# Kernel optimization log

Measured on AMD Instinct MI355X. Metric: run time of the kernel, lower is better.

Reference implementation:

```python
import jax, jax.numpy as jnp
import numpy as np

B, C_IN, C_OUT, N, MODES = 16, 128, 128, 16384, 128

def setup_inputs() -> dict:
    key = jax.random.key(0)
    k1, k2, k3, k4 = jax.random.split(key, 4)
    scale = 1.0 / (C_IN * C_OUT)
    x = jax.random.normal(k1, (B, C_IN, N), dtype=jnp.float32)
    wbases = jax.random.normal(k2, (N, MODES), dtype=jnp.float32)
    bases = jax.random.normal(k3, (N, MODES), dtype=jnp.float32)
    W = scale * jax.random.uniform(k4, (C_IN, C_OUT, MODES), dtype=jnp.float32)
    return {"x": x, "wbases": wbases, "bases": bases, "W": W}

def reference(x, wbases, bases, W):
    # project onto weighted bases: [B, C_in, N] x [N, K] -> [B, C_in, K]
    x_co = jnp.einsum('bcx,xk->bck', x, wbases)
    # per-mode channel mixing: [B, C_in, K] x [C_in, C_out, K] -> [B, C_out, K]
    x_hat = jnp.einsum('bik,iok->bok', x_co, W)
    # reconstruct: [B, C_out, K] x [N, K] -> [B, C_out, N]
    return jnp.einsum('bok,xk->box', x_hat, bases)
```

## Files before the change

### kernel.cpp

```cpp
#include <hip/hip_runtime.h>
#include <hip/hip_bf16.h>
#include <stdint.h>

#define NB 16
#define NC 128
#define NK 128
#define NSP 16384
#define SPLIT 32
#define CHUNK 512
#define BK 64

typedef float f32x4 __attribute__((ext_vector_type(4)));
typedef __bf16 bf16x8 __attribute__((ext_vector_type(8)));

__device__ __forceinline__ unsigned short f32_to_bf16(float a) {
  unsigned int u = __float_as_uint(a);
  return (unsigned short)((u + 0x7fffu + ((u >> 16) & 1u)) >> 16);
}

__device__ __forceinline__ unsigned int pack_bf16(float a, float b) {
  unsigned int ua = __float_as_uint(a);
  unsigned int ub = __float_as_uint(b);
  ua = (ua + 0x7fffu + ((ua >> 16) & 1u)) >> 16;
  ub = (ub + 0x7fffu + ((ub >> 16) & 1u)) & 0xffff0000u;
  return ua | ub;
}

__device__ __forceinline__ bf16x8 pack8(float4 a0, float4 a1) {
  uint4 u;
  u.x = pack_bf16(a0.x, a0.y);
  u.y = pack_bf16(a0.z, a0.w);
  u.z = pack_bf16(a1.x, a1.y);
  u.w = pack_bf16(a1.z, a1.w);
  return __builtin_bit_cast(bf16x8, u);
}

__global__ void k0_prep(const float* __restrict__ wb, unsigned short* __restrict__ wbT,
                        const float* __restrict__ bases, unsigned short* __restrict__ bb) {
  __shared__ float tile[32][33];
  if (blockIdx.x < 2048) {
    int bid = blockIdx.x;
    int kt = (bid & 3) * 32;
    int nt = (bid >> 2) * 32;
    int tx = threadIdx.x & 31;
    int ty = threadIdx.x >> 5;
#pragma unroll
    for (int i = 0; i < 32; i += 8)
      tile[ty + i][tx] = wb[(size_t)(nt + ty + i) * NK + kt + tx];
    __syncthreads();
#pragma unroll
    for (int i = 0; i < 32; i += 8)
      wbT[(size_t)(kt + ty + i) * NSP + nt + tx] = f32_to_bf16(tile[tx][ty + i]);
  } else {
    int i = (blockIdx.x - 2048) * 256 + threadIdx.x;
    float4 v = ((const float4*)bases)[i];
    uint2 o;
    o.x = pack_bf16(v.x, v.y);
    o.y = pack_bf16(v.z, v.w);
    ((uint2*)bb)[i] = o;
  }
}

__global__ __launch_bounds__(256, 4)
void k1_proj(const float* __restrict__ x, const unsigned short* __restrict__ wbT,
             float* __restrict__ part) {
  int blk = blockIdx.x;
  int khalf = blk >> 9;
  int b = (blk >> 5) & 15;
  int chunk = blk & 31;
  int n0 = chunk * CHUNK;
  int tid = threadIdx.x;
  int lane = tid & 63;
  int wave = tid >> 6;
  int cb = (wave & 1) * 64;
  int kb = khalf * 64 + (wave >> 1) * 32;
  int r = lane & 15;
  int q = lane >> 4;

  f32x4 acc[4][2];
#pragma unroll
  for (int t = 0; t < 4; ++t)
#pragma unroll
    for (int u = 0; u < 2; ++u) acc[t][u] = (f32x4){0.f, 0.f, 0.f, 0.f};

  const float* xrow = x + (size_t)(b * NC + cb + r) * NSP + n0;
  const unsigned short* wrow = wbT + (size_t)(kb + r) * NSP + n0;

#pragma unroll 2
  for (int it = 0; it < CHUNK / BK; ++it) {
#pragma unroll
    for (int s = 0; s < 2; ++s) {
      int c2 = it * BK + s * 32 + q * 8;
      bf16x8 af[4], bf[2];
#pragma unroll
      for (int t = 0; t < 4; ++t) {
        const float4* p = (const float4*)(xrow + (size_t)t * 16 * NSP + c2);
        af[t] = pack8(p[0], p[1]);
      }
#pragma unroll
      for (int u = 0; u < 2; ++u)
        bf[u] = *(const bf16x8*)(wrow + (size_t)u * 16 * NSP + c2);
#pragma unroll
      for (int t = 0; t < 4; ++t)
#pragma unroll
        for (int u = 0; u < 2; ++u)
          acc[t][u] = __builtin_amdgcn_mfma_f32_16x16x32_bf16(af[t], bf[u],
                                                              acc[t][u], 0, 0, 0);
    }
  }

  float* pp = part + (size_t)(b * SPLIT + chunk) * (NC * NK);
  int rq = q * 4;
#pragma unroll
  for (int t = 0; t < 4; ++t)
#pragma unroll
    for (int u = 0; u < 2; ++u)
#pragma unroll
      for (int v = 0; v < 4; ++v)
        pp[(cb + 16 * t + rq + v) * NK + kb + 16 * u + r] = acc[t][u][v];
}

__global__ __launch_bounds__(256)
void k1b_reduce(const float* __restrict__ part, float* __restrict__ x_co) {
  int idx = blockIdx.x * 256 + threadIdx.x;
  int b = idx >> 13;
  int r2 = idx & 8191;
  const float2* p = (const float2*)(part + (size_t)b * SPLIT * (NC * NK)) + r2;
  float2 s = {0.f, 0.f};
#pragma unroll
  for (int c = 0; c < SPLIT; ++c) {
    float2 v = p[(size_t)c * (NC * NK / 2)];
    s.x += v.x;
    s.y += v.y;
  }
  ((float2*)x_co)[idx] = s;
}

__global__ __launch_bounds__(128)
void k2_mix(const float* __restrict__ x_co, const float* __restrict__ W,
            unsigned short* __restrict__ xhat_bf) {
  int b = blockIdx.x >> 6;
  int o0 = (blockIdx.x & 63) * 2;
  int k = threadIdx.x;
  const float* xc = x_co + (size_t)b * NC * NK + k;
  const float* w0 = W + (size_t)o0 * NK + k;
  float a0 = 0.f, a1 = 0.f;
#pragma unroll 4
  for (int i = 0; i < NC; ++i) {
    float v = xc[(size_t)i * NK];
    a0 += v * w0[(size_t)i * (NC * NK)];
    a1 += v * w0[(size_t)i * (NC * NK) + NK];
  }
  size_t base = ((size_t)b * NC + o0) * NK + k;
  xhat_bf[base] = f32_to_bf16(a0);
  xhat_bf[base + NK] = f32_to_bf16(a1);
}

__global__ __launch_bounds__(256, 4)
void k3_recon(const unsigned short* __restrict__ xhat_bf,
              const unsigned short* __restrict__ bases_bf,
              float* __restrict__ out) {
  int blk = blockIdx.x;
  int mo0 = (blk & 15) * 128;
  int n0 = (blk >> 4) * 256;
  int tid = threadIdx.x;
  int lane = tid & 63;
  int wave = tid >> 6;
  int mb = (wave & 1) * 64;
  int nb = (wave >> 1) * 64;
  int r = lane & 15;
  int q = lane >> 4;
  int rq = q * 4;

  const unsigned short* arow = xhat_bf + (size_t)(mo0 + mb + r) * NK + q * 8;

#pragma unroll
  for (int sub = 0; sub < 2; ++sub) {
    const unsigned short* brow =
        bases_bf + (size_t)(n0 + sub * 128 + nb + r) * NK + q * 8;
    f32x4 acc[4][4];
#pragma unroll
    for (int t = 0; t < 4; ++t)
#pragma unroll
      for (int u = 0; u < 4; ++u) acc[t][u] = (f32x4){0.f, 0.f, 0.f, 0.f};
#pragma unroll
    for (int s = 0; s < 4; ++s) {
      bf16x8 af[4], bf[4];
#pragma unroll
      for (int t = 0; t < 4; ++t)
        af[t] = *(const bf16x8*)(arow + (size_t)t * 16 * NK + s * 32);
#pragma unroll
      for (int u = 0; u < 4; ++u)
        bf[u] = *(const bf16x8*)(brow + (size_t)u * 16 * NK + s * 32);
#pragma unroll
      for (int t = 0; t < 4; ++t)
#pragma unroll
        for (int u = 0; u < 4; ++u)
          acc[t][u] = __builtin_amdgcn_mfma_f32_16x16x32_bf16(af[t], bf[u],
                                                              acc[t][u], 0, 0, 0);
    }
    float* obase = out + (size_t)(mo0 + mb + rq) * NSP + n0 + sub * 128 + nb + r;
#pragma unroll
    for (int t = 0; t < 4; ++t)
#pragma unroll
      for (int u = 0; u < 4; ++u)
#pragma unroll
        for (int v = 0; v < 4; ++v)
          obase[(size_t)(16 * t + v) * NSP + 16 * u] = acc[t][u][v];
  }
}

extern "C" void kernel_launch(void* const* d_in, const int* in_sizes, int n_in,
                              void* d_out, int out_size, void* d_ws, size_t ws_size,
                              hipStream_t stream) {
  const float* x = (const float*)d_in[0];
  const float* wbases = (const float*)d_in[1];
  const float* bases = (const float*)d_in[2];
  const float* W = (const float*)d_in[3];
  float* out = (float*)d_out;

  char* ws = (char*)d_ws;
  if (ws_size < ((size_t)42 << 20)) return;
  unsigned short* wbT = (unsigned short*)(ws);
  unsigned short* bases_bf = (unsigned short*)(ws + ((size_t)4 << 20));
  float* part = (float*)(ws + ((size_t)8 << 20));
  float* x_co = (float*)(ws + ((size_t)40 << 20));
  unsigned short* xhat_bf = (unsigned short*)(ws + ((size_t)41 << 20));

  k0_prep<<<4096, 256, 0, stream>>>(wbases, wbT, bases, bases_bf);
  k1_proj<<<1024, 256, 0, stream>>>(x, wbT, part);
  k1b_reduce<<<512, 256, 0, stream>>>(part, x_co);
  k2_mix<<<NB * NC / 2, 128, 0, stream>>>(x_co, W, xhat_bf);
  k3_recon<<<1024, 256, 0, stream>>>(xhat_bf, bases_bf, out);
}
```

Measured before the change: 360.7 us.

## Stage k1 projection tiles through double-buffered LDS via direct global-to-LDS loads

Reworks the projection kernel so each block covers half the input channels and all 128 modes, so the x data is read once instead of twice across mode halves. Tiles of x (fp32, XOR-swizzled) and bf16 wbases are copied into a double-buffered LDS area with global_load_lds, and the next tile is prefetched while MFMAs run on the current one. The change adds a block barrier every 32-element step and converts fp32 to bf16 when reading from LDS. It also uses 32KB of LDS per block, which may reduce occupancy.

```diff
diff --git a/kernel.cpp b/kernel.cpp
--- a/kernel.cpp
+++ b/kernel.cpp
@@ -8,7 +8,6 @@
 #define NSP 16384
 #define SPLIT 32
 #define CHUNK 512
-#define BK 64
 
 typedef float f32x4 __attribute__((ext_vector_type(4)));
 typedef __bf16 bf16x8 __attribute__((ext_vector_type(8)));
@@ -33,6 +32,12 @@
   u.z = pack_bf16(a1.x, a1.y);
   u.w = pack_bf16(a1.z, a1.w);
   return __builtin_bit_cast(bf16x8, u);
+}
+
+__device__ __forceinline__ void gl_lds16(const void* g, void* l) {
+  __builtin_amdgcn_global_load_lds(
+      (const __attribute__((address_space(1))) unsigned int*)g,
+      (__attribute__((address_space(3))) unsigned int*)l, 16, 0, 0);
 }
 
 __global__ void k0_prep(const float* __restrict__ wb, unsigned short* __restrict__ wbT,
@@ -65,59 +70,86 @@
 void k1_proj(const float* __restrict__ x, const unsigned short* __restrict__ wbT,
              float* __restrict__ part) {
   int blk = blockIdx.x;
-  int khalf = blk >> 9;
-  int b = (blk >> 5) & 15;
   int chunk = blk & 31;
+  int bc = blk >> 5;
+  int b = bc >> 1;
+  int chalf = bc & 1;
   int n0 = chunk * CHUNK;
+  __shared__ __align__(16) char lds[2][16384];
   int tid = threadIdx.x;
   int lane = tid & 63;
   int wave = tid >> 6;
-  int cb = (wave & 1) * 64;
-  int kb = khalf * 64 + (wave >> 1) * 32;
+  int cbw = (wave & 1) * 32;
+  int kbw = (wave >> 1) * 64;
   int r = lane & 15;
   int q = lane >> 4;
 
-  f32x4 acc[4][2];
-#pragma unroll
-  for (int t = 0; t < 4; ++t)
-#pragma unroll
-    for (int u = 0; u < 2; ++u) acc[t][u] = (f32x4){0.f, 0.f, 0.f, 0.f};
-
-  const float* xrow = x + (size_t)(b * NC + cb + r) * NSP + n0;
-  const unsigned short* wrow = wbT + (size_t)(kb + r) * NSP + n0;
+  f32x4 acc[2][4];
+#pragma unroll
+  for (int t = 0; t < 2; ++t)
+#pragma unroll
+    for (int u = 0; u < 4; ++u) acc[t][u] = (f32x4){0.f, 0.f, 0.f, 0.f};
+
+  const float* aptr = x + (size_t)(b * NC + chalf * 64 + (lane >> 3)) * NSP +
+                      n0 + ((lane & 7) ^ (lane >> 3)) * 4;
+  const unsigned short* bptr =
+      wbT + (size_t)(lane >> 2) * NSP + n0 + (lane & 3) * 8;
+
+#pragma unroll
+  for (int j = 0; j < 2; ++j) {
+    int i = wave * 2 + j;
+    gl_lds16(aptr + (size_t)(8 * i) * NSP, lds[0] + i * 1024);
+    gl_lds16(bptr + (size_t)(16 * i) * NSP, lds[0] + 8192 + i * 1024);
+  }
+  __syncthreads();
 
 #pragma unroll 2
-  for (int it = 0; it < CHUNK / BK; ++it) {
-#pragma unroll
-    for (int s = 0; s < 2; ++s) {
-      int c2 = it * BK + s * 32 + q * 8;
-      bf16x8 af[4], bf[2];
-#pragma unroll
-      for (int t = 0; t < 4; ++t) {
-        const float4* p = (const float4*)(xrow + (size_t)t * 16 * NSP + c2);
-        af[t] = pack8(p[0], p[1]);
+  for (int it = 0; it < CHUNK / 32; ++it) {
+    int cur = it & 1;
+    if (it + 1 < CHUNK / 32) {
+#pragma unroll
+      for (int j = 0; j < 2; ++j) {
+        int i = wave * 2 + j;
+        gl_lds16(aptr + (size_t)(8 * i) * NSP + (it + 1) * 32,
+                 lds[cur ^ 1] + i * 1024);
+        gl_lds16(bptr + (size_t)(16 * i) * NSP + (it + 1) * 32,
+                 lds[cur ^ 1] + 8192 + i * 1024);
       }
-#pragma unroll
-      for (int u = 0; u < 2; ++u)
-        bf[u] = *(const bf16x8*)(wrow + (size_t)u * 16 * NSP + c2);
-#pragma unroll
-      for (int t = 0; t < 4; ++t)
-#pragma unroll
-        for (int u = 0; u < 2; ++u)
-          acc[t][u] = __builtin_amdgcn_mfma_f32_16x16x32_bf16(af[t], bf[u],
-                                                              acc[t][u], 0, 0, 0);
-    }
+    }
+    const char* La = lds[cur];
+    const char* Lb = lds[cur] + 8192;
+    bf16x8 af[2], bf[4];
+#pragma unroll
+    for (int t = 0; t < 2; ++t) {
+      int rw = cbw + 16 * t + r;
+      float4 f0 = *(const float4*)(La + rw * 128 + (((2 * q + 0) ^ (r & 7)) << 4));
+      float4 f1 = *(const float4*)(La + rw * 128 + (((2 * q + 1) ^ (r & 7)) << 4));
+      af[t] = pack8(f0, f1);
+    }
+#pragma unroll
+    for (int u = 0; u < 4; ++u) {
+      int rk = kbw + 16 * u + r;
+      bf[u] = *(const bf16x8*)(Lb + rk * 64 + q * 16);
+    }
+#pragma unroll
+    for (int t = 0; t < 2; ++t)
+#pragma unroll
+      for (int u = 0; u < 4; ++u)
+        acc[t][u] = __builtin_amdgcn_mfma_f32_16x16x32_bf16(af[t], bf[u],
+                                                            acc[t][u], 0, 0, 0);
+    __syncthreads();
   }
 
   float* pp = part + (size_t)(b * SPLIT + chunk) * (NC * NK);
   int rq = q * 4;
 #pragma unroll
-  for (int t = 0; t < 4; ++t)
-#pragma unroll
-    for (int u = 0; u < 2; ++u)
+  for (int t = 0; t < 2; ++t)
+#pragma unroll
+    for (int u = 0; u < 4; ++u)
 #pragma unroll
       for (int v = 0; v < 4; ++v)
-        pp[(cb + 16 * t + rq + v) * NK + kb + 16 * u + r] = acc[t][u][v];
+        pp[(chalf * 64 + cbw + 16 * t + rq + v) * NK + kbw + 16 * u + r] =
+            acc[t][u][v];
 }
 
 __global__ __launch_bounds__(256)
```

Result: faster. 324.2 us (-10.1%).
